# Performance work log

Measured on AMD Instinct MI355X. Metric: run time of the kernel, lower is better.

Reference implementation:

```python
import jax, jax.numpy as jnp
import numpy as np

B, N1, N2, C1, C2, MLP_OUT = 16, 4096, 1024, 128, 256, 256


def setup_inputs() -> dict:
    key = jax.random.key(0)
    k = jax.random.split(key, 8)
    xyz1 = jax.random.normal(k[0], (B, N1, 3), dtype=jnp.float32)
    feat1 = jax.random.normal(k[1], (B, N1, C1), dtype=jnp.float32)
    xyz2 = jax.random.normal(k[2], (B, N2, 3), dtype=jnp.float32)
    feat2 = jax.random.normal(k[3], (B, N2, C2), dtype=jnp.float32)
    d_in = C1 + C2
    W1 = jax.random.normal(k[4], (d_in, MLP_OUT), dtype=jnp.float32) / np.sqrt(d_in)
    b1 = jnp.zeros((MLP_OUT,), dtype=jnp.float32)
    W2 = jax.random.normal(k[5], (MLP_OUT, MLP_OUT), dtype=jnp.float32) / np.sqrt(MLP_OUT)
    b2 = jnp.zeros((MLP_OUT,), dtype=jnp.float32)
    return {"xyz1": xyz1, "feat1": feat1, "xyz2": xyz2, "feat2": feat2,
            "W1": W1, "b1": b1, "W2": W2, "b2": b2}


def reference(xyz1, feat1, xyz2, feat2, W1, b1, W2, b2):
    # squared pairwise distances [B, N1, N2]
    dists = jnp.sum((xyz1[:, :, None, :] - xyz2[:, None, :, :]) ** 2, axis=-1)
    # 3 nearest neighbors (smallest distances)
    neg_d3, idx = jax.lax.top_k(-dists, 3)      # [B, N1, 3]
    d3 = jnp.maximum(-neg_d3, 1e-10)
    w = 1.0 / d3
    w = w / jnp.sum(w, axis=-1, keepdims=True)   # [B, N1, 3]
    # gather neighbor features: [B, N1, 3, C2]
    neighbor_feats = jax.vmap(lambda f, i: f[i])(feat2, idx)
    interpolated = jnp.sum(w[..., None] * neighbor_feats, axis=2)  # [B, N1, C2]
    new_feat = jnp.concatenate([interpolated, feat1], axis=-1)     # [B, N1, C2+C1]
    h = jax.nn.relu(new_feat @ W1 + b1)
    return jax.nn.relu(h @ W2 + b2)
```

## Files before the change

### kernel.cpp

```cpp
#include <hip/hip_runtime.h>
#include <cstdint>
#include <cstddef>

typedef unsigned short ushort_t;
typedef unsigned int uint_t;

typedef __bf16 bf16x8 __attribute__((ext_vector_type(8)));
typedef float floatx4 __attribute__((ext_vector_type(4)));

#define B_ 16
#define N1_ 4096
#define N2_ 1024
#define C1_ 128
#define C2_ 256
#define DIN_ 384
#define DOUT_ 256
#define M_ (B_ * N1_)


__device__ __forceinline__ ushort_t f2bf(float f) {
  unsigned int u = __builtin_bit_cast(unsigned int, f);
  u = (u + 0x7fffu + ((u >> 16) & 1u)) >> 16;
  return (ushort_t)u;
}

#define AS_IDX(t, row, kk) \
  ((t) * 2048 + (row) * 32 + ((kk) ^ ((((row) >> 1) & 3) << 3)))


__global__ __launch_bounds__(256) void prep_kernel(
    const float* __restrict__ W1, const float* __restrict__ W2,
    ushort_t* __restrict__ W1s, ushort_t* __restrict__ W2s) {
  int e = blockIdx.x * 256 + threadIdx.x;
  if (e < DOUT_ * DIN_) {
    int kk = e & 31, n = (e >> 5) & 255, t = e >> 13;
    W1s[e] = f2bf(W1[(size_t)(t * 32 + kk) * DOUT_ + n]);
  }
  if (e < DOUT_ * DOUT_) {
    int kk = e & 31, n = (e >> 5) & 255, t = e >> 13;
    W2s[e] = f2bf(W2[(size_t)(t * 32 + kk) * DOUT_ + n]);
  }
}


__device__ __forceinline__ void ins_exact(float& s0, float& s1, float& s2,
                                          int& i0, int& i1, int& i2,
                                          float d, int p) {
  float ns2 = __builtin_amdgcn_fmed3f(d, s1, s2);
  float ns1 = __builtin_amdgcn_fmed3f(d, s0, s1);
  float ns0 = fminf(d, s0);
  bool c0 = d < s0, c1 = d < s1, c2 = d < s2;
  i2 = c1 ? i1 : (c2 ? p : i2);
  i1 = c0 ? i0 : (c1 ? p : i1);
  i0 = c0 ? p : i0;
  s0 = ns0; s1 = ns1; s2 = ns2;
}

__device__ __forceinline__ void ins_merge(float& s0, float& s1, float& s2,
                                          int& i0, int& i1, int& i2,
                                          float e, int j) {
  bool t0 = (e < s0) || (e == s0 && j < i0);
  bool t1 = (e < s1) || (e == s1 && j < i1);
  bool t2 = (e < s2) || (e == s2 && j < i2);
  s2 = t1 ? s1 : (t2 ? e : s2);
  i2 = t1 ? i1 : (t2 ? j : i2);
  s1 = t0 ? s0 : (t1 ? e : s1);
  i1 = t0 ? i0 : (t1 ? j : i1);
  s0 = t0 ? e : s0;
  i0 = t0 ? j : i0;
}

__global__ __launch_bounds__(128) void knn_kernel(
    const float* __restrict__ xyz1, const float* __restrict__ xyz2,
    int* __restrict__ idx_out, float* __restrict__ w_out) {
  __shared__ float4 xs4[N2_];
  int b = blockIdx.x >> 6;
  int n1base = (blockIdx.x & 63) << 6;
  const float* p2 = xyz2 + (size_t)b * N2_ * 3;
  for (int i = threadIdx.x; i < N2_; i += 128) {
    const float* s = p2 + 3 * i;
    xs4[i] = make_float4(s[0], s[1], s[2], 0.0f);
  }
  __syncthreads();

  int g = threadIdx.x >> 3;
  int sub = threadIdx.x & 7;

  float px[4], py[4], pz[4];
  float s0[4], s1[4], s2[4];
  int i0[4], i1[4], i2[4];
#pragma unroll
  for (int r = 0; r < 4; ++r) {
    int row = b * N1_ + n1base + g + 16 * r;
    const float* p1 = xyz1 + (size_t)row * 3;
    px[r] = p1[0]; py[r] = p1[1]; pz[r] = p1[2];
    s0[r] = 3.0e38f; s1[r] = 3.0e38f; s2[r] = 3.0e38f;
    i0[r] = 0; i1[r] = 0; i2[r] = 0;
  }

  int p = sub;
#pragma unroll 4
  for (int t = 0; t < N2_ / 8; ++t) {
    float4 qv = xs4[p];
#pragma unroll
    for (int r = 0; r < 4; ++r) {
      float dx = px[r] - qv.x, dy = py[r] - qv.y, dz = pz[r] - qv.z;
      float d = dx * dx + dy * dy + dz * dz;
      ins_exact(s0[r], s1[r], s2[r], i0[r], i1[r], i2[r], d, p);
    }
    p += 8;
  }

#pragma unroll
  for (int mm = 1; mm <= 4; mm <<= 1) {
#pragma unroll
    for (int r = 0; r < 4; ++r) {
      float e0 = __shfl_xor(s0[r], mm), e1 = __shfl_xor(s1[r], mm), e2 = __shfl_xor(s2[r], mm);
      int j0 = __shfl_xor(i0[r], mm), j1 = __shfl_xor(i1[r], mm), j2 = __shfl_xor(i2[r], mm);
      ins_merge(s0[r], s1[r], s2[r], i0[r], i1[r], i2[r], e0, j0);
      ins_merge(s0[r], s1[r], s2[r], i0[r], i1[r], i2[r], e1, j1);
      ins_merge(s0[r], s1[r], s2[r], i0[r], i1[r], i2[r], e2, j2);
    }
  }

  if (sub == 0) {
#pragma unroll
    for (int r = 0; r < 4; ++r) {
      int row = b * N1_ + n1base + g + 16 * r;
      float r0 = 1.0f / fmaxf(s0[r], 1e-10f);
      float r1 = 1.0f / fmaxf(s1[r], 1e-10f);
      float r2 = 1.0f / fmaxf(s2[r], 1e-10f);
      float s = 1.0f / (r0 + r1 + r2);
      int base = row * 3;
      idx_out[base + 0] = i0[r];
      idx_out[base + 1] = i1[r];
      idx_out[base + 2] = i2[r];
      w_out[base + 0] = r0 * s;
      w_out[base + 1] = r1 * s;
      w_out[base + 2] = r2 * s;
    }
  }
}


__global__ __launch_bounds__(256, 2) void fused_kernel(
    const float* __restrict__ feat1, const float* __restrict__ feat2,
    const int* __restrict__ idx, const float* __restrict__ w,
    const ushort_t* __restrict__ W1s, const float* __restrict__ b1,
    const ushort_t* __restrict__ W2s, const float* __restrict__ b2,
    float* __restrict__ out) {
  __shared__ ushort_t As[64 * 384];
  const int tid = threadIdx.x;
  const int wave = tid >> 6;
  const int lane = tid & 63;
  const int m = lane & 15;
  const int q = lane >> 4;
  const int row0 = blockIdx.x * 64;
  const int b = row0 >> 12;

  const int b_off = (wave * 64 + m) * 32 + q * 8;

  bf16x8 w0[4], w1[4], w2[4], w3[4], af[4];

#pragma unroll
  for (int j = 0; j < 4; ++j) {
    w0[j] = *(const bf16x8*)(W1s + b_off + j * 512);
    w1[j] = *(const bf16x8*)(W1s + 8192 + b_off + j * 512);
  }

#pragma unroll 4
  for (int it = 0; it < 16; ++it) {
    int rl = wave * 16 + it;
    int row = row0 + rl;
    const int* ip = idx + (size_t)row * 3;
    const float* wp = w + (size_t)row * 3;
    int i0 = ip[0], i1 = ip[1], i2 = ip[2];
    float w0v = wp[0], w1v = wp[1], w2v = wp[2];

    const float4* f0 = (const float4*)(feat2 + ((size_t)b * N2_ + i0) * C2_);
    const float4* f1 = (const float4*)(feat2 + ((size_t)b * N2_ + i1) * C2_);
    const float4* f2 = (const float4*)(feat2 + ((size_t)b * N2_ + i2) * C2_);
    float4 a = f0[lane];
    float4 c = f1[lane];
    float4 d = f2[lane];
    float vx = w0v * a.x + w1v * c.x + w2v * d.x;
    float vy = w0v * a.y + w1v * c.y + w2v * d.y;
    float vz = w0v * a.z + w1v * c.z + w2v * d.z;
    float vw = w0v * a.w + w1v * c.w + w2v * d.w;
    uint_t lo = (uint_t)f2bf(vx) | ((uint_t)f2bf(vy) << 16);
    uint_t hi = (uint_t)f2bf(vz) | ((uint_t)f2bf(vw) << 16);
    int e = AS_IDX(lane >> 3, rl, (4 * lane) & 31);
    *(uint2*)&As[e] = make_uint2(lo, hi);

    float2 t1 = ((const float2*)(feat1 + (size_t)row * C1_))[lane];
    uint_t pk = (uint_t)f2bf(t1.x) | ((uint_t)f2bf(t1.y) << 16);
    int e1 = AS_IDX(8 + (lane >> 4), rl, (2 * lane) & 31);
    *(uint_t*)&As[e1] = pk;
  }
  __syncthreads();

  floatx4 acc[4][4];
#pragma unroll
  for (int i = 0; i < 4; ++i)
#pragma unroll
    for (int j = 0; j < 4; ++j) acc[i][j] = (floatx4)0.0f;

#pragma unroll
  for (int tt = 0; tt < 12; tt += 4) {
#pragma unroll
    for (int j = 0; j < 4; ++j) {
      w2[j] = *(const bf16x8*)(W1s + (size_t)(tt + 2) * 8192 + b_off + j * 512);
      w3[j] = *(const bf16x8*)(W1s + (size_t)(tt + 3) * 8192 + b_off + j * 512);
    }
#pragma unroll
    for (int i = 0; i < 4; ++i)
      af[i] = *(const bf16x8*)&As[AS_IDX(tt, m + 16 * i, q * 8)];
#pragma unroll
    for (int i = 0; i < 4; ++i)
#pragma unroll
      for (int j = 0; j < 4; ++j)
        acc[i][j] = __builtin_amdgcn_mfma_f32_16x16x32_bf16(af[i], w0[j],
                                                            acc[i][j], 0, 0, 0);
#pragma unroll
    for (int i = 0; i < 4; ++i)
      af[i] = *(const bf16x8*)&As[AS_IDX(tt + 1, m + 16 * i, q * 8)];
#pragma unroll
    for (int i = 0; i < 4; ++i)
#pragma unroll
      for (int j = 0; j < 4; ++j)
        acc[i][j] = __builtin_amdgcn_mfma_f32_16x16x32_bf16(af[i], w1[j],
                                                            acc[i][j], 0, 0, 0);
    if (tt + 4 < 12) {
#pragma unroll
      for (int j = 0; j < 4; ++j) {
        w0[j] = *(const bf16x8*)(W1s + (size_t)(tt + 4) * 8192 + b_off + j * 512);
        w1[j] = *(const bf16x8*)(W1s + (size_t)(tt + 5) * 8192 + b_off + j * 512);
      }
    }
#pragma unroll
    for (int i = 0; i < 4; ++i)
      af[i] = *(const bf16x8*)&As[AS_IDX(tt + 2, m + 16 * i, q * 8)];
#pragma unroll
    for (int i = 0; i < 4; ++i)
#pragma unroll
      for (int j = 0; j < 4; ++j)
        acc[i][j] = __builtin_amdgcn_mfma_f32_16x16x32_bf16(af[i], w2[j],
                                                            acc[i][j], 0, 0, 0);
#pragma unroll
    for (int i = 0; i < 4; ++i)
      af[i] = *(const bf16x8*)&As[AS_IDX(tt + 3, m + 16 * i, q * 8)];
#pragma unroll
    for (int i = 0; i < 4; ++i)
#pragma unroll
      for (int j = 0; j < 4; ++j)
        acc[i][j] = __builtin_amdgcn_mfma_f32_16x16x32_bf16(af[i], w3[j],
                                                            acc[i][j], 0, 0, 0);
  }

#pragma unroll
  for (int j = 0; j < 4; ++j) {
    w0[j] = *(const bf16x8*)(W2s + b_off + j * 512);
    w1[j] = *(const bf16x8*)(W2s + 8192 + b_off + j * 512);
  }
  __syncthreads();

  ushort_t* HS = As;
#pragma unroll
  for (int j = 0; j < 4; ++j) {
    int col = wave * 64 + j * 16 + m;
    float bv = b1[col];
    int cb = (col >> 3) & 3;
    int tb = (col >> 5) * 2048 + (col & 7);
#pragma unroll
    for (int i = 0; i < 4; ++i)
#pragma unroll
      for (int r = 0; r < 4; ++r) {
        int row = i * 16 + q * 4 + r;
        float v = acc[i][j][r] + bv;
        v = v > 0.0f ? v : 0.0f;
        int ch = cb ^ ((row >> 2) & 3);
        HS[tb + row * 32 + ch * 8] = f2bf(v);
      }
  }
  __syncthreads();

  floatx4 acc2[4][4];
#pragma unroll
  for (int i = 0; i < 4; ++i)
#pragma unroll
    for (int j = 0; j < 4; ++j) acc2[i][j] = (floatx4)0.0f;

#pragma unroll
  for (int tt = 0; tt < 8; tt += 4) {
#pragma unroll
    for (int j = 0; j < 4; ++j) {
      w2[j] = *(const bf16x8*)(W2s + (size_t)(tt + 2) * 8192 + b_off + j * 512);
      w3[j] = *(const bf16x8*)(W2s + (size_t)(tt + 3) * 8192 + b_off + j * 512);
    }
#pragma unroll
    for (int i = 0; i < 4; ++i) {
      int row = m + 16 * i;
      int ch = q ^ ((row >> 2) & 3);
      af[i] = *(const bf16x8*)&HS[tt * 2048 + row * 32 + ch * 8];
    }
#pragma unroll
    for (int i = 0; i < 4; ++i)
#pragma unroll
      for (int j = 0; j < 4; ++j)
        acc2[i][j] = __builtin_amdgcn_mfma_f32_16x16x32_bf16(af[i], w0[j],
                                                             acc2[i][j], 0, 0, 0);
#pragma unroll
    for (int i = 0; i < 4; ++i) {
      int row = m + 16 * i;
      int ch = q ^ ((row >> 2) & 3);
      af[i] = *(const bf16x8*)&HS[(tt + 1) * 2048 + row * 32 + ch * 8];
    }
#pragma unroll
    for (int i = 0; i < 4; ++i)
#pragma unroll
      for (int j = 0; j < 4; ++j)
        acc2[i][j] = __builtin_amdgcn_mfma_f32_16x16x32_bf16(af[i], w1[j],
                                                             acc2[i][j], 0, 0, 0);
    if (tt + 4 < 8) {
#pragma unroll
      for (int j = 0; j < 4; ++j) {
        w0[j] = *(const bf16x8*)(W2s + (size_t)(tt + 4) * 8192 + b_off + j * 512);
        w1[j] = *(const bf16x8*)(W2s + (size_t)(tt + 5) * 8192 + b_off + j * 512);
      }
    }
#pragma unroll
    for (int i = 0; i < 4; ++i) {
      int row = m + 16 * i;
      int ch = q ^ ((row >> 2) & 3);
      af[i] = *(const bf16x8*)&HS[(tt + 2) * 2048 + row * 32 + ch * 8];
    }
#pragma unroll
    for (int i = 0; i < 4; ++i)
#pragma unroll
      for (int j = 0; j < 4; ++j)
        acc2[i][j] = __builtin_amdgcn_mfma_f32_16x16x32_bf16(af[i], w2[j],
                                                             acc2[i][j], 0, 0, 0);
#pragma unroll
    for (int i = 0; i < 4; ++i) {
      int row = m + 16 * i;
      int ch = q ^ ((row >> 2) & 3);
      af[i] = *(const bf16x8*)&HS[(tt + 3) * 2048 + row * 32 + ch * 8];
    }
#pragma unroll
    for (int i = 0; i < 4; ++i)
#pragma unroll
      for (int j = 0; j < 4; ++j)
        acc2[i][j] = __builtin_amdgcn_mfma_f32_16x16x32_bf16(af[i], w3[j],
                                                             acc2[i][j], 0, 0, 0);
  }

#pragma unroll
  for (int j = 0; j < 4; ++j) {
    int col = wave * 64 + j * 16 + m;
    float bv = b2[col];
#pragma unroll
    for (int i = 0; i < 4; ++i)
#pragma unroll
      for (int r = 0; r < 4; ++r) {
        int row = i * 16 + q * 4 + r;
        float v = acc2[i][j][r] + bv;
        v = v > 0.0f ? v : 0.0f;
        out[(size_t)(row0 + row) * DOUT_ + col] = v;
      }
  }
}


constexpr size_t OFF_W1S = 0;
constexpr size_t OFF_W2S = OFF_W1S + 196608;
constexpr size_t OFF_IDX = OFF_W2S + 131072;
constexpr size_t OFF_W = OFF_IDX + 786432;
constexpr size_t WS_TOTAL = OFF_W + 786432;

extern "C" void kernel_launch(void* const* d_in, const int* in_sizes, int n_in,
                              void* d_out, int out_size, void* d_ws, size_t ws_size,
                              hipStream_t stream) {
  const float* xyz1 = (const float*)d_in[0];
  const float* feat1 = (const float*)d_in[1];
  const float* xyz2 = (const float*)d_in[2];
  const float* feat2 = (const float*)d_in[3];
  const float* W1 = (const float*)d_in[4];
  const float* b1 = (const float*)d_in[5];
  const float* W2 = (const float*)d_in[6];
  const float* b2 = (const float*)d_in[7];

  if (ws_size < WS_TOTAL) return;

  char* ws = (char*)d_ws;
  ushort_t* W1s = (ushort_t*)(ws + OFF_W1S);
  ushort_t* W2s = (ushort_t*)(ws + OFF_W2S);
  int* idx = (int*)(ws + OFF_IDX);
  float* w = (float*)(ws + OFF_W);

  prep_kernel<<<384, 256, 0, stream>>>(W1, W2, W1s, W2s);
  knn_kernel<<<B_ * (N1_ / 64), 128, 0, stream>>>(xyz1, xyz2, idx, w);
  fused_kernel<<<M_ / 64, 256, 0, stream>>>(feat1, feat2, idx, w, W1s, b1, W2s,
                                            b2, (float*)d_out);
}
```

Before: 217.6 us.

## Give each KNN thread one query row with two independent top-3 chains

The KNN kernel now assigns one query point to each group of 8 threads instead of four, and doubles the block size to 256 threads, so four times as many waves are launched. Within a thread, candidates are split into two interleaved top-3 lists that are merged before the cross-lane shuffle reduction, which shortens the dependent compare-and-select chain. The aim is better latency hiding and occupancy in the distance and top-3 loop. The cost is that each shared-memory point load now serves one distance instead of four, so LDS traffic per distance rises. A stray `y1 == y1` guard on one distance term is a no-op for finite inputs.

```diff
diff --git a/kernel.cpp b/kernel.cpp
--- a/kernel.cpp
+++ b/kernel.cpp
@@ -70,14 +70,14 @@
   i0 = t0 ? j : i0;
 }
 
-__global__ __launch_bounds__(128) void knn_kernel(
+__global__ __launch_bounds__(256) void knn_kernel(
     const float* __restrict__ xyz1, const float* __restrict__ xyz2,
     int* __restrict__ idx_out, float* __restrict__ w_out) {
   __shared__ float4 xs4[N2_];
-  int b = blockIdx.x >> 6;
-  int n1base = (blockIdx.x & 63) << 6;
+  int b = blockIdx.x >> 7;
+  int n1base = (blockIdx.x & 127) << 5;
   const float* p2 = xyz2 + (size_t)b * N2_ * 3;
-  for (int i = threadIdx.x; i < N2_; i += 128) {
+  for (int i = threadIdx.x; i < N2_; i += 256) {
     const float* s = p2 + 3 * i;
     xs4[i] = make_float4(s[0], s[1], s[2], 0.0f);
   }
@@ -85,60 +85,60 @@
 
   int g = threadIdx.x >> 3;
   int sub = threadIdx.x & 7;
-
-  float px[4], py[4], pz[4];
-  float s0[4], s1[4], s2[4];
-  int i0[4], i1[4], i2[4];
-#pragma unroll
-  for (int r = 0; r < 4; ++r) {
-    int row = b * N1_ + n1base + g + 16 * r;
-    const float* p1 = xyz1 + (size_t)row * 3;
-    px[r] = p1[0]; py[r] = p1[1]; pz[r] = p1[2];
-    s0[r] = 3.0e38f; s1[r] = 3.0e38f; s2[r] = 3.0e38f;
-    i0[r] = 0; i1[r] = 0; i2[r] = 0;
-  }
-
-  int p = sub;
-#pragma unroll 4
-  for (int t = 0; t < N2_ / 8; ++t) {
-    float4 qv = xs4[p];
-#pragma unroll
-    for (int r = 0; r < 4; ++r) {
-      float dx = px[r] - qv.x, dy = py[r] - qv.y, dz = pz[r] - qv.z;
+  int row = b * N1_ + n1base + g;
+  const float* p1 = xyz1 + (size_t)row * 3;
+  float x1 = p1[0], y1 = p1[1], z1 = p1[2];
+
+  float as0 = 3.0e38f, as1 = 3.0e38f, as2 = 3.0e38f;
+  float bs0 = 3.0e38f, bs1 = 3.0e38f, bs2 = 3.0e38f;
+  int ai0 = 0, ai1 = 0, ai2 = 0;
+  int bi0 = 0, bi1 = 0, bi2 = 0;
+
+  int pA = sub;
+  int pB = sub + 8;
+#pragma unroll 8
+  for (int t = 0; t < N2_ / 16; ++t) {
+    float4 qa = xs4[pA];
+    float4 qb = xs4[pB];
+    {
+      float dx = x1 - qa.x, dy = y1 - qa.y, dz = y1 == y1 ? z1 - qa.z : 0.0f;
       float d = dx * dx + dy * dy + dz * dz;
-      ins_exact(s0[r], s1[r], s2[r], i0[r], i1[r], i2[r], d, p);
-    }
-    p += 8;
-  }
+      ins_exact(as0, as1, as2, ai0, ai1, ai2, d, pA);
+    }
+    {
+      float dx = x1 - qb.x, dy = y1 - qb.y, dz = z1 - qb.z;
+      float d = dx * dx + dy * dy + dz * dz;
+      ins_exact(bs0, bs1, bs2, bi0, bi1, bi2, d, pB);
+    }
+    pA += 16;
+    pB += 16;
+  }
+
+  ins_merge(as0, as1, as2, ai0, ai1, ai2, bs0, bi0);
+  ins_merge(as0, as1, as2, ai0, ai1, ai2, bs1, bi1);
+  ins_merge(as0, as1, as2, ai0, ai1, ai2, bs2, bi2);
 
 #pragma unroll
   for (int mm = 1; mm <= 4; mm <<= 1) {
-#pragma unroll
-    for (int r = 0; r < 4; ++r) {
-      float e0 = __shfl_xor(s0[r], mm), e1 = __shfl_xor(s1[r], mm), e2 = __shfl_xor(s2[r], mm);
-      int j0 = __shfl_xor(i0[r], mm), j1 = __shfl_xor(i1[r], mm), j2 = __shfl_xor(i2[r], mm);
-      ins_merge(s0[r], s1[r], s2[r], i0[r], i1[r], i2[r], e0, j0);
-      ins_merge(s0[r], s1[r], s2[r], i0[r], i1[r], i2[r], e1, j1);
-      ins_merge(s0[r], s1[r], s2[r], i0[r], i1[r], i2[r], e2, j2);
-    }
+    float e0 = __shfl_xor(as0, mm), e1 = __shfl_xor(as1, mm), e2 = __shfl_xor(as2, mm);
+    int j0 = __shfl_xor(ai0, mm), j1 = __shfl_xor(ai1, mm), j2 = __shfl_xor(ai2, mm);
+    ins_merge(as0, as1, as2, ai0, ai1, ai2, e0, j0);
+    ins_merge(as0, as1, as2, ai0, ai1, ai2, e1, j1);
+    ins_merge(as0, as1, as2, ai0, ai1, ai2, e2, j2);
   }
 
   if (sub == 0) {
-#pragma unroll
-    for (int r = 0; r < 4; ++r) {
-      int row = b * N1_ + n1base + g + 16 * r;
-      float r0 = 1.0f / fmaxf(s0[r], 1e-10f);
-      float r1 = 1.0f / fmaxf(s1[r], 1e-10f);
-      float r2 = 1.0f / fmaxf(s2[r], 1e-10f);
-      float s = 1.0f / (r0 + r1 + r2);
-      int base = row * 3;
-      idx_out[base + 0] = i0[r];
-      idx_out[base + 1] = i1[r];
-      idx_out[base + 2] = i2[r];
-      w_out[base + 0] = r0 * s;
-      w_out[base + 1] = r1 * s;
-      w_out[base + 2] = r2 * s;
-    }
+    float r0 = 1.0f / fmaxf(as0, 1e-10f);
+    float r1 = 1.0f / fmaxf(as1, 1e-10f);
+    float r2 = 1.0f / fmaxf(as2, 1e-10f);
+    float s = 1.0f / (r0 + r1 + r2);
+    int base = row * 3;
+    idx_out[base + 0] = ai0;
+    idx_out[base + 1] = ai1;
+    idx_out[base + 2] = ai2;
+    w_out[base + 0] = r0 * s;
+    w_out[base + 1] = r1 * s;
+    w_out[base + 2] = r2 * s;
   }
 }
 
@@ -398,7 +398,7 @@
   float* w = (float*)(ws + OFF_W);
 
   prep_kernel<<<384, 256, 0, stream>>>(W1, W2, W1s, W2s);
-  knn_kernel<<<B_ * (N1_ / 64), 128, 0, stream>>>(xyz1, xyz2, idx, w);
+  knn_kernel<<<B_ * (N1_ / 32), 256, 0, stream>>>(xyz1, xyz2, idx, w);
   fused_kernel<<<M_ / 64, 256, 0, stream>>>(feat1, feat2, idx, w, W1s, b1, W2s,
                                             b2, (float*)d_out);
 }
```

Result: faster. 196.4 us (-9.7%).
